# Kernel optimization log

Measured on AMD Instinct MI355X. Metric: run time of the kernel, lower is better.

## Reference

```python
import jax, jax.numpy as jnp
import numpy as np


def setup_inputs() -> dict:
    key = jax.random.key(0)
    k1, k2 = jax.random.split(key)
    s = jax.random.normal(k1, (8192, 512), dtype=jnp.float32)
    t = jax.random.normal(k2, (8192, 512), dtype=jnp.float32)
    return {"s": s, "t": t}


def reference(s, t):
    # Pairwise squared Euclidean distance: dist[i, j] = ||t[j] - s[i]||^2
    # Expressed via the identity ||s||^2 + ||t||^2 - 2 s @ t^T to avoid
    # materializing the [n, q, d] broadcast intermediate of the original.
    s_sq = jnp.sum(s * s, axis=1)  # [n]
    t_sq = jnp.sum(t * t, axis=1)  # [q]
    cross = jnp.einsum('nd,qd->nq', s, t)  # [n, q]
    dist = s_sq[:, None] + t_sq[None, :] - 2.0 * cross
    return dist
```

## Files before the change

kernel.cpp:

```cpp
#include <hip/hip_runtime.h>
#include <hip/hip_bf16.h>
#include <stdint.h>


typedef __attribute__((ext_vector_type(8))) short short8v;
typedef __attribute__((ext_vector_type(4))) float f32x4;

static __device__ __forceinline__ unsigned short f32_to_bf16_rne(float f) {
    unsigned int u = __float_as_uint(f);
    unsigned int lsb = (u >> 16) & 1u;
    u += 0x7fffu + lsb;
    return (unsigned short)(u >> 16);
}

static __device__ __forceinline__ void async_load16(const void* g, void* l) {
    __builtin_amdgcn_global_load_lds(
        (const __attribute__((address_space(1))) void*)g,
        (__attribute__((address_space(3))) void*)l,
        16, 0, 0);
}

__global__ __launch_bounds__(256) void prep_kernel(const float* __restrict__ x,
                                                   unsigned short* __restrict__ xb,
                                                   float* __restrict__ nrm,
                                                   float scale) {
    const int tid  = threadIdx.x;
    const int wid  = tid >> 6;
    const int lane = tid & 63;
    const int row  = blockIdx.x * 4 + wid;
    const float* xr = x + (size_t)row * 512;

    float4 v0 = ((const float4*)xr)[lane * 2 + 0];
    float4 v1 = ((const float4*)xr)[lane * 2 + 1];

    float ss = v0.x * v0.x + v0.y * v0.y + v0.z * v0.z + v0.w * v0.w
             + v1.x * v1.x + v1.y * v1.y + v1.z * v1.z + v1.w * v1.w;
#pragma unroll
    for (int off = 32; off > 0; off >>= 1) ss += __shfl_down(ss, off, 64);
    if (lane == 0) nrm[row] = ss;

    unsigned short u[8];
    float vals[8] = {v0.x, v0.y, v0.z, v0.w, v1.x, v1.y, v1.z, v1.w};
#pragma unroll
    for (int e = 0; e < 8; ++e) u[e] = f32_to_bf16_rne(vals[e] * scale);
    unsigned int w0 = (unsigned)u[0] | ((unsigned)u[1] << 16);
    unsigned int w1 = (unsigned)u[2] | ((unsigned)u[3] << 16);
    unsigned int w2 = (unsigned)u[4] | ((unsigned)u[5] << 16);
    unsigned int w3 = (unsigned)u[6] | ((unsigned)u[7] << 16);
    uint4 pk = make_uint4(w0, w1, w2, w3);
    ((uint4*)(xb + (size_t)row * 512))[lane] = pk;
}

#define TILE 128
#define BK 32

__global__ __launch_bounds__(256) void dist_mfma(const unsigned short* __restrict__ sb,
                                                 const unsigned short* __restrict__ tb,
                                                 const float* __restrict__ ssq,
                                                 const float* __restrict__ tsq,
                                                 float* __restrict__ out,
                                                 int N, int Q, int D) {
    __shared__ unsigned short lds_a[TILE * BK];
    __shared__ unsigned short lds_b[TILE * BK];

    const int tid  = threadIdx.x;
    const int wid  = tid >> 6;
    const int lane = tid & 63;
    const int quad = lane >> 4;
    const int r    = lane & 15;

    const int bid = blockIdx.x;
    const int nBm = N / TILE, nBn = Q / TILE;
    int bm, bn;
    if ((nBm & 7) == 0 && (nBn & 7) == 0) {
        const int super = bid >> 6, within = bid & 63;
        const int spr = nBn >> 3;
        const int sm = super / spr, sn = super % spr;
        bm = (sm << 3) + (within >> 3);
        bn = (sn << 3) + (within & 7);
    } else {
        bm = bid / nBn;
        bn = bid - bm * nBn;
    }

    const int m_w = (wid & 1) * 64;
    const int n_w = (wid >> 1) * 64;

    f32x4 acc[4][4];
#pragma unroll
    for (int a = 0; a < 4; ++a)
#pragma unroll
        for (int b = 0; b < 4; ++b) acc[a][b] = (f32x4){0.f, 0.f, 0.f, 0.f};

    const int c    = tid;
    const int srow = c >> 2;
    const int skb  = (c & 3) << 3;
    const unsigned short* gA = sb + (size_t)(bm * TILE + srow) * D + skb;
    const unsigned short* gB = tb + (size_t)(bn * TILE + srow) * D + skb;
    unsigned short* lA = lds_a + wid * 512;
    unsigned short* lB = lds_b + wid * 512;
    const size_t half_g = (size_t)64 * D;

    for (int k0 = 0; k0 < D; k0 += BK) {
        __syncthreads();
        async_load16(gA + k0,          lA);
        async_load16(gA + k0 + half_g, lA + 2048);
        async_load16(gB + k0,          lB);
        async_load16(gB + k0 + half_g, lB + 2048);
        __syncthreads();

        short8v aF[4], bF[4];
#pragma unroll
        for (int im = 0; im < 4; ++im)
            aF[im] = *(const short8v*)(lds_a + (m_w + im * 16 + r) * BK + quad * 8);
#pragma unroll
        for (int in = 0; in < 4; ++in)
            bF[in] = *(const short8v*)(lds_b + (n_w + in * 16 + r) * BK + quad * 8);
#pragma unroll
        for (int im = 0; im < 4; ++im)
#pragma unroll
            for (int in = 0; in < 4; ++in)
                acc[im][in] = __builtin_amdgcn_mfma_f32_16x16x32_bf16(
                    aF[im], bF[in], acc[im][in], 0, 0, 0);
    }

    const int gm = bm * TILE + m_w;
    const int gn = bn * TILE + n_w;
    float tq[4];
#pragma unroll
    for (int in = 0; in < 4; ++in) tq[in] = tsq[gn + in * 16 + r];
#pragma unroll
    for (int im = 0; im < 4; ++im) {
#pragma unroll
        for (int j = 0; j < 4; ++j) {
            const int i = gm + im * 16 + quad * 4 + j;
            const float sv = ssq[i];
            float* orow = out + (size_t)i * (size_t)Q + gn;
#pragma unroll
            for (int in = 0; in < 4; ++in)
                orow[in * 16 + r] = sv + tq[in] + acc[im][in][j];
        }
    }
}

__global__ void dist_fallback(const float* __restrict__ s, const float* __restrict__ t,
                              float* __restrict__ out, int N, int Q, int D) {
    __shared__ float ls[16][17], lt[16][17];
    const int tj = threadIdx.x, ti = threadIdx.y;
    const int i = blockIdx.y * 16 + ti, j = blockIdx.x * 16 + tj;
    float cross = 0.f, ssq = 0.f, tsq = 0.f;
    for (int k0 = 0; k0 < D; k0 += 16) {
        __syncthreads();
        ls[ti][tj] = s[(size_t)(blockIdx.y * 16 + ti) * D + k0 + tj];
        lt[ti][tj] = t[(size_t)(blockIdx.x * 16 + ti) * D + k0 + tj];
        __syncthreads();
#pragma unroll
        for (int kk = 0; kk < 16; ++kk) {
            float a = ls[ti][kk], b = lt[tj][kk];
            cross += a * b; ssq += a * a; tsq += b * b;
        }
    }
    out[(size_t)i * Q + j] = ssq + tsq - 2.f * cross;
}

extern "C" void kernel_launch(void* const* d_in, const int* in_sizes, int n_in,
                              void* d_out, int out_size, void* d_ws, size_t ws_size,
                              hipStream_t stream) {
    const float* s = (const float*)d_in[0];
    const float* t = (const float*)d_in[1];
    float* out = (float*)d_out;
    const int D = 512;
    const int N = in_sizes[0] / D;
    const int Q = in_sizes[1] / D;

    const size_t need = ((size_t)N + (size_t)Q) * D * sizeof(unsigned short)
                      + ((size_t)N + (size_t)Q) * sizeof(float);

    if (ws_size >= need && D == 512 && (N % TILE) == 0 && (Q % TILE) == 0) {
        unsigned short* sb = (unsigned short*)d_ws;
        unsigned short* tb = sb + (size_t)N * D;
        float* ssq = (float*)(tb + (size_t)Q * D);
        float* tsq = ssq + N;
        prep_kernel<<<N / 4, 256, 0, stream>>>(s, sb, ssq, -2.0f);
        prep_kernel<<<Q / 4, 256, 0, stream>>>(t, tb, tsq, 1.0f);
        const int blocks = (N / TILE) * (Q / TILE);
        dist_mfma<<<blocks, 256, 0, stream>>>(sb, tb, ssq, tsq, out, N, Q, D);
    } else {
        dim3 g(Q / 16, N / 16), b(16, 16);
        dist_fallback<<<g, b, 0, stream>>>(s, t, out, N, Q, D);
    }
}
```

Baseline: 372.3 us.

## Double K-tile depth, XOR-swizzle LDS layout, and use nontemporal output stores

```diff
diff --git a/kernel.cpp b/kernel.cpp
--- a/kernel.cpp
+++ b/kernel.cpp
@@ -52,7 +52,7 @@
 }
 
 #define TILE 128
-#define BK 32
+#define BK 64
 
 __global__ __launch_bounds__(256) void dist_mfma(const unsigned short* __restrict__ sb,
                                                  const unsigned short* __restrict__ tb,
@@ -92,36 +92,52 @@
 #pragma unroll
         for (int b = 0; b < 4; ++b) acc[a][b] = (f32x4){0.f, 0.f, 0.f, 0.f};
 
-    const int c    = tid;
-    const int srow = c >> 2;
-    const int skb  = (c & 3) << 3;
-    const unsigned short* gA = sb + (size_t)(bm * TILE + srow) * D + skb;
-    const unsigned short* gB = tb + (size_t)(bn * TILE + srow) * D + skb;
-    unsigned short* lA = lds_a + wid * 512;
-    unsigned short* lB = lds_b + wid * 512;
-    const size_t half_g = (size_t)64 * D;
+    const unsigned short* gA[4];
+    const unsigned short* gB[4];
+    unsigned short* lA[4];
+    unsigned short* lB[4];
+#pragma unroll
+    for (int i = 0; i < 4; ++i) {
+        const int p    = i * 256 + tid;
+        const int row  = p >> 3;
+        const int gch  = (tid & 7) ^ (row & 7);
+        gA[i] = sb + (size_t)(bm * TILE + row) * D + gch * 8;
+        gB[i] = tb + (size_t)(bn * TILE + row) * D + gch * 8;
+        lA[i] = lds_a + (i * 256 + wid * 64) * 8;
+        lB[i] = lds_b + (i * 256 + wid * 64) * 8;
+    }
 
     for (int k0 = 0; k0 < D; k0 += BK) {
         __syncthreads();
-        async_load16(gA + k0,          lA);
-        async_load16(gA + k0 + half_g, lA + 2048);
-        async_load16(gB + k0,          lB);
-        async_load16(gB + k0 + half_g, lB + 2048);
-        __syncthreads();
-
-        short8v aF[4], bF[4];
-#pragma unroll
-        for (int im = 0; im < 4; ++im)
-            aF[im] = *(const short8v*)(lds_a + (m_w + im * 16 + r) * BK + quad * 8);
-#pragma unroll
-        for (int in = 0; in < 4; ++in)
-            bF[in] = *(const short8v*)(lds_b + (n_w + in * 16 + r) * BK + quad * 8);
-#pragma unroll
-        for (int im = 0; im < 4; ++im)
-#pragma unroll
-            for (int in = 0; in < 4; ++in)
-                acc[im][in] = __builtin_amdgcn_mfma_f32_16x16x32_bf16(
-                    aF[im], bF[in], acc[im][in], 0, 0, 0);
+#pragma unroll
+        for (int i = 0; i < 4; ++i) {
+            async_load16(gA[i] + k0, lA[i]);
+            async_load16(gB[i] + k0, lB[i]);
+        }
+        __syncthreads();
+
+#pragma unroll
+        for (int ks = 0; ks < 2; ++ks) {
+            short8v aF[4], bF[4];
+#pragma unroll
+            for (int im = 0; im < 4; ++im) {
+                const int row = m_w + im * 16 + r;
+                const int cp  = (ks * 4 + quad) ^ (row & 7);
+                aF[im] = *(const short8v*)(lds_a + row * BK + cp * 8);
+            }
+#pragma unroll
+            for (int in = 0; in < 4; ++in) {
+                const int row = n_w + in * 16 + r;
+                const int cp  = (ks * 4 + quad) ^ (row & 7);
+                bF[in] = *(const short8v*)(lds_b + row * BK + cp * 8);
+            }
+#pragma unroll
+            for (int im = 0; im < 4; ++im)
+#pragma unroll
+                for (int in = 0; in < 4; ++in)
+                    acc[im][in] = __builtin_amdgcn_mfma_f32_16x16x32_bf16(
+                        aF[im], bF[in], acc[im][in], 0, 0, 0);
+        }
     }
 
     const int gm = bm * TILE + m_w;
@@ -138,7 +154,8 @@
             float* orow = out + (size_t)i * (size_t)Q + gn;
 #pragma unroll
             for (int in = 0; in < 4; ++in)
-                orow[in * 16 + r] = sv + tq[in] + acc[im][in][j];
+                __builtin_nontemporal_store(sv + tq[in] + acc[im][in][j],
+                                            &orow[in * 16 + r]);
         }
     }
 }
```

Result: faster. 349.8 us (-6.0%).
